# Optimization experiments

Measured on AMD Instinct MI355X. Metric: run time of the kernel, lower is better.

Reference implementation:

```python
import jax, jax.numpy as jnp
import numpy as np

N = 50000
E = 800000
D_IN = 128
D_HID = 128
D_OUT = 128
EPS = 1e-5


def setup_inputs() -> dict:
    key = jax.random.key(0)
    ks = jax.random.split(key, 10)
    x = jax.random.normal(ks[0], (N, D_IN), dtype=jnp.float32)
    edge_index = jax.random.randint(ks[1], (2, E), 0, N, dtype=jnp.int64)
    def lin(k, fi, fo):
        return jax.random.normal(k, (fi, fo), dtype=jnp.float32) / jnp.sqrt(jnp.float32(fi))
    return {
        "x": x,
        "edge_index": edge_index,
        "W1": lin(ks[2], D_IN, D_HID), "b1": jnp.zeros((D_HID,), jnp.float32),
        "W2": lin(ks[3], D_HID, D_HID), "b2": jnp.zeros((D_HID,), jnp.float32),
        "W3": lin(ks[4], D_HID, D_OUT), "b3": jnp.zeros((D_OUT,), jnp.float32),
        "g1": jnp.ones((D_HID,), jnp.float32), "be1": jnp.zeros((D_HID,), jnp.float32),
        "g2": jnp.ones((D_HID,), jnp.float32), "be2": jnp.zeros((D_HID,), jnp.float32),
    }


def _gcn_conv(x, src, dst, norm, W, b):
    # x' = D^{-1/2}(A+I)D^{-1/2} X W + b  (PyG GCNConv with self-loops)
    h = x @ W                              # [N, F]
    msgs = h[src] * norm[:, None]          # [E+N, F] gather
    agg = jax.ops.segment_sum(msgs, dst, num_segments=x.shape[0])  # scatter-add
    return agg + b


def _batchnorm(x, gamma, beta):
    mu = jnp.mean(x, axis=0)
    var = jnp.mean((x - mu) ** 2, axis=0)  # biased var, as in torch BN
    return (x - mu) * jax.lax.rsqrt(var + EPS) * gamma + beta


def reference(x, edge_index, W1, b1, W2, b2, W3, b3, g1, be1, g2, be2):
    n = x.shape[0]
    loops = jnp.arange(n, dtype=edge_index.dtype)
    src = jnp.concatenate([edge_index[0], loops])
    dst = jnp.concatenate([edge_index[1], loops])
    deg = jax.ops.segment_sum(jnp.ones_like(dst, dtype=x.dtype), dst, num_segments=n)
    dinv = jnp.where(deg > 0, jax.lax.rsqrt(deg), 0.0)
    norm = dinv[src] * dinv[dst]           # [E+N]

    h = _gcn_conv(x, src, dst, norm, W1, b1)
    h = jax.nn.relu(_batchnorm(h, g1, be1))
    h = _gcn_conv(h, src, dst, norm, W2, b2)
    h = jax.nn.relu(_batchnorm(h, g2, be2))
    h = _gcn_conv(h, src, dst, norm, W3, b3)
    # F.normalize(p=2, dim=-1)
    return h / jnp.maximum(jnp.linalg.norm(h, axis=-1, keepdims=True), 1e-12)
```

## Files before the change

### kernel.cpp

```cpp
#include <hip/hip_runtime.h>
#include <hip/hip_bf16.h>

#define D 128

typedef __bf16 bf16x8 __attribute__((ext_vector_type(8)));
typedef float floatx4 __attribute__((ext_vector_type(4)));


__global__ void k_count(const int* __restrict__ dst, int E, int* __restrict__ cnt) {
    int e = blockIdx.x * blockDim.x + threadIdx.x;
    if (e < E) atomicAdd(&cnt[dst[e]], 1);
}

__global__ __launch_bounds__(256) void k_scan1(const int* __restrict__ cnt, int n,
                                               int* __restrict__ bsum) {
    int i = blockIdx.x * 256 + threadIdx.x;
    int x = (i < n) ? cnt[i] : 0;
    #pragma unroll
    for (int off = 32; off > 0; off >>= 1) x += __shfl_xor(x, off, 64);
    __shared__ int ws[4];
    if ((threadIdx.x & 63) == 0) ws[threadIdx.x >> 6] = x;
    __syncthreads();
    if (threadIdx.x == 0) bsum[blockIdx.x] = ws[0] + ws[1] + ws[2] + ws[3];
}

__global__ void k_scan2(const int* __restrict__ bsum, int nb, int* __restrict__ boff) {
    int t = threadIdx.x;
    int lane = t & 63, wid = t >> 6;
    int x = (t < nb) ? bsum[t] : 0;
    int incl = x;
    #pragma unroll
    for (int off = 1; off < 64; off <<= 1) {
        int y = __shfl_up(incl, off, 64);
        if (lane >= off) incl += y;
    }
    __shared__ int ws[4];
    if (lane == 63) ws[wid] = incl;
    __syncthreads();
    int o = 0;
    for (int w = 0; w < wid; w++) o += ws[w];
    if (t < nb) boff[t] = o + incl - x;
}

__global__ __launch_bounds__(256) void k_scan3(const int* __restrict__ cnt,
                                               const int* __restrict__ boff, int n, int E,
                                               int* __restrict__ row_ptr, int* __restrict__ cursor,
                                               float* __restrict__ dinv) {
    int t = threadIdx.x;
    int lane = t & 63, wid = t >> 6;
    int i = blockIdx.x * 256 + t;
    int x = (i < n) ? cnt[i] : 0;
    int incl = x;
    #pragma unroll
    for (int off = 1; off < 64; off <<= 1) {
        int y = __shfl_up(incl, off, 64);
        if (lane >= off) incl += y;
    }
    __shared__ int ws[4];
    if (lane == 63) ws[wid] = incl;
    __syncthreads();
    int o = boff[blockIdx.x];
    for (int w = 0; w < wid; w++) o += ws[w];
    if (i < n) {
        int excl = o + incl - x;
        row_ptr[i] = excl;
        cursor[i] = excl;
        dinv[i] = rsqrtf((float)(x + 1));
    }
    if (blockIdx.x == 0 && t == 0) row_ptr[n] = E;
}

__global__ __launch_bounds__(256) void k_fill(const int* __restrict__ src,
                                              const int* __restrict__ dst, int E,
                                              int* __restrict__ cursor,
                                              unsigned short* __restrict__ esrc, int n) {
    int rs = (n + 7) >> 3;
    int lo = blockIdx.y * rs, hi = lo + rs;
    int step = gridDim.x * 256;
    for (int e = blockIdx.x * 256 + threadIdx.x; e < E; e += step) {
        int d = dst[e];
        int s = src[e];
        if (d >= lo && d < hi) {
            int p = atomicAdd(&cursor[d], 1);
            esrc[p] = (unsigned short)s;
        }
    }
}


__global__ __launch_bounds__(256) void k_prepw(const float* __restrict__ W1,
                                               const float* __restrict__ W2,
                                               const float* __restrict__ W3,
                                               unsigned short* __restrict__ Wt) {
    const float* W = (blockIdx.x == 0) ? W1 : (blockIdx.x == 1) ? W2 : W3;
    unsigned short* o = Wt + blockIdx.x * 16384;
    for (int i = threadIdx.x; i < 16384; i += 256) {
        int k = i >> 7, nn = i & 127;
        __hip_bfloat16 h = __float2bfloat16(W[i]);
        o[nn * 128 + k] = *(unsigned short*)&h;
    }
}


__global__ __launch_bounds__(256) void k_gemm(
    const float* __restrict__ X, const unsigned short* __restrict__ Wt,
    const float* __restrict__ scale, const float* __restrict__ stats_in,
    const float* __restrict__ gamma, const float* __restrict__ beta,
    float* __restrict__ stats_zero,
    unsigned* __restrict__ hs, int n, float invN) {
    __shared__ unsigned short Wl[128 * 128];
    __shared__ float bnl[256];
    int t = threadIdx.x;
    if (stats_in && t < 128) {
        float s = stats_in[t] + stats_in[256 + t] + stats_in[512 + t] + stats_in[768 + t];
        float q = stats_in[128 + t] + stats_in[384 + t] + stats_in[640 + t] + stats_in[896 + t];
        float mean = s * invN;
        float var = q * invN - mean * mean;
        float a = gamma[t] * rsqrtf(var + 1e-5f);
        bnl[t] = a;
        bnl[128 + t] = beta[t] - mean * a;
    }
    if (stats_zero && blockIdx.x == 0) {
        stats_zero[t] = 0.f;
        stats_zero[256 + t] = 0.f;
        stats_zero[512 + t] = 0.f;
        stats_zero[768 + t] = 0.f;
    }
    {
        const uint4* wg = (const uint4*)Wt;
        uint4* wl4 = (uint4*)Wl;
        #pragma unroll
        for (int j = 0; j < 8; j++) {
            int idx = j * 256 + t;
            int nn = idx >> 4, lc = idx & 15;
            wl4[nn * 16 + (lc ^ (nn & 15))] = wg[idx];
        }
    }
    __syncthreads();

    int l = t & 63, w = t >> 6;
    int lm = l & 15, quad = l >> 4;
    int m = blockIdx.x * 64 + w * 16 + lm;
    int rm = (m < n) ? m : (n - 1);
    const float* xrow = X + (size_t)rm * D;

    floatx4 acc[8];
    #pragma unroll
    for (int nt = 0; nt < 8; nt++) acc[nt] = (floatx4){0.f, 0.f, 0.f, 0.f};

    #pragma unroll
    for (int ks = 0; ks < 4; ks++) {
        int k0 = ks * 32 + quad * 8;
        float4 xa = *(const float4*)(xrow + k0);
        float4 xb = *(const float4*)(xrow + k0 + 4);
        if (stats_in) {
            float4 a0 = *(const float4*)&bnl[k0];
            float4 a1 = *(const float4*)&bnl[k0 + 4];
            float4 c0 = *(const float4*)&bnl[128 + k0];
            float4 c1 = *(const float4*)&bnl[128 + k0 + 4];
            xa.x = fmaxf(xa.x * a0.x + c0.x, 0.f);
            xa.y = fmaxf(xa.y * a0.y + c0.y, 0.f);
            xa.z = fmaxf(xa.z * a0.z + c0.z, 0.f);
            xa.w = fmaxf(xa.w * a0.w + c0.w, 0.f);
            xb.x = fmaxf(xb.x * a1.x + c1.x, 0.f);
            xb.y = fmaxf(xb.y * a1.y + c1.y, 0.f);
            xb.z = fmaxf(xb.z * a1.z + c1.z, 0.f);
            xb.w = fmaxf(xb.w * a1.w + c1.w, 0.f);
        }
        bf16x8 xf;
        xf[0] = (__bf16)xa.x; xf[1] = (__bf16)xa.y;
        xf[2] = (__bf16)xa.z; xf[3] = (__bf16)xa.w;
        xf[4] = (__bf16)xb.x; xf[5] = (__bf16)xb.y;
        xf[6] = (__bf16)xb.z; xf[7] = (__bf16)xb.w;
        int pc = (ks * 4 + quad) ^ lm;
        #pragma unroll
        for (int nt = 0; nt < 8; nt++) {
            const bf16x8 wf = *(const bf16x8*)&Wl[(nt * 16 + lm) * 128 + pc * 8];
            acc[nt] = __builtin_amdgcn_mfma_f32_16x16x32_bf16(wf, xf, acc[nt], 0, 0, 0);
        }
    }

    float s = scale[rm];
    if (m < n) {
        #pragma unroll
        for (int nt = 0; nt < 8; nt++) {
            __hip_bfloat16 h0 = __float2bfloat16(acc[nt][0] * s);
            __hip_bfloat16 h1 = __float2bfloat16(acc[nt][1] * s);
            __hip_bfloat16 h2 = __float2bfloat16(acc[nt][2] * s);
            __hip_bfloat16 h3 = __float2bfloat16(acc[nt][3] * s);
            uint2 uu;
            uu.x = (unsigned)*(unsigned short*)&h0 | ((unsigned)*(unsigned short*)&h1 << 16);
            uu.y = (unsigned)*(unsigned short*)&h2 | ((unsigned)*(unsigned short*)&h3 << 16);
            *(uint2*)&hs[((size_t)(nt >> 1) * n + m) * 16 + (nt & 1) * 8 + quad * 2] = uu;
        }
    }
}


__device__ inline float2 bf2f(unsigned u) {
    union { unsigned i; float f; } lo, hi;
    lo.i = u << 16;
    hi.i = u & 0xffff0000u;
    float2 r; r.x = lo.f; r.y = hi.f; return r;
}

__global__ __launch_bounds__(256) void k_agg(
    const unsigned* __restrict__ hs, const int* __restrict__ row_ptr,
    const unsigned short* __restrict__ esrc, const float* __restrict__ dinv,
    const float* __restrict__ bias, float* __restrict__ out,
    float* __restrict__ stats4, int n, int mode) {
    __shared__ float lsS[16][32];
    __shared__ float lsQ[16][32];
    int t = threadIdx.x;
    int grp = t >> 4, sub = t & 15;
    int qd = sub >> 2;
    int qe = sub & 3;
    int bid = blockIdx.x;
    int p = (bid >> 1) & 3;
    int nblk = (bid >> 3) * 2 + (bid & 1);
    const unsigned* hsp = hs + (size_t)p * n * 16;

    lsS[t >> 5][t & 31] = 0.f;
    lsS[(t >> 5) + 8][t & 31] = 0.f;
    lsQ[t >> 5][t & 31] = 0.f;
    lsQ[(t >> 5) + 8][t & 31] = 0.f;
    __syncthreads();

    float4 bA = *(const float4*)&bias[p * 32 + qe * 8];
    float4 bB = *(const float4*)&bias[p * 32 + qe * 8 + 4];

    int node0 = nblk * 64 + grp * 4;
    int rp[5];
    #pragma unroll
    for (int k = 0; k < 5; k++) {
        int ik = node0 + k;
        if (ik > n) ik = n;
        rp[k] = row_ptr[ik];
    }

    #pragma unroll
    for (int ni = 0; ni < 4; ni++) {
        int node = node0 + ni;
        if (node >= n) break;
        int beg = rp[ni], end = rp[ni + 1];
        float sc = dinv[node];
        int e_cur = (beg + sub < end) ? (int)esrc[beg + sub] : 0;
        uint4 sv = *(const uint4*)&hsp[(size_t)node * 16 + qe * 4];
        float2 a0 = bf2f(qd == 0 ? sv.x : 0u);
        float2 a1 = bf2f(qd == 0 ? sv.y : 0u);
        float2 a2 = bf2f(qd == 0 ? sv.z : 0u);
        float2 a3 = bf2f(qd == 0 ? sv.w : 0u);

        for (int base = beg; base < end; base += 16) {
            int mm = end - base;
            if (mm > 16) mm = 16;
            int e_nxt = (base + 16 + sub < end) ? (int)esrc[base + 16 + sub] : 0;
            int u0, u1, u2, u3;
            float w0, w1, w2, w3;
            {
                int ei = qd;
                int ix = ei < mm ? ei : mm - 1;
                u0 = __shfl(e_cur, ix, 16);
                w0 = ei < mm ? 1.f : 0.f;
            }
            {
                int ei = 4 + qd;
                int ix = ei < mm ? ei : mm - 1;
                u1 = __shfl(e_cur, ix, 16);
                w1 = ei < mm ? 1.f : 0.f;
            }
            {
                int ei = 8 + qd;
                int ix = ei < mm ? ei : mm - 1;
                u2 = __shfl(e_cur, ix, 16);
                w2 = ei < mm ? 1.f : 0.f;
            }
            {
                int ei = 12 + qd;
                int ix = ei < mm ? ei : mm - 1;
                u3 = __shfl(e_cur, ix, 16);
                w3 = ei < mm ? 1.f : 0.f;
            }
            uint4 g0 = *(const uint4*)&hsp[(size_t)u0 * 16 + qe * 4];
            uint4 g1 = *(const uint4*)&hsp[(size_t)u1 * 16 + qe * 4];
            uint4 g2 = *(const uint4*)&hsp[(size_t)u2 * 16 + qe * 4];
            uint4 g3 = *(const uint4*)&hsp[(size_t)u3 * 16 + qe * 4];
            float2 v;
            v = bf2f(g0.x); a0.x = fmaf(v.x, w0, a0.x); a0.y = fmaf(v.y, w0, a0.y);
            v = bf2f(g0.y); a1.x = fmaf(v.x, w0, a1.x); a1.y = fmaf(v.y, w0, a1.y);
            v = bf2f(g0.z); a2.x = fmaf(v.x, w0, a2.x); a2.y = fmaf(v.y, w0, a2.y);
            v = bf2f(g0.w); a3.x = fmaf(v.x, w0, a3.x); a3.y = fmaf(v.y, w0, a3.y);
            v = bf2f(g1.x); a0.x = fmaf(v.x, w1, a0.x); a0.y = fmaf(v.y, w1, a0.y);
            v = bf2f(g1.y); a1.x = fmaf(v.x, w1, a1.x); a1.y = fmaf(v.y, w1, a1.y);
            v = bf2f(g1.z); a2.x = fmaf(v.x, w1, a2.x); a2.y = fmaf(v.y, w1, a2.y);
            v = bf2f(g1.w); a3.x = fmaf(v.x, w1, a3.x); a3.y = fmaf(v.y, w1, a3.y);
            v = bf2f(g2.x); a0.x = fmaf(v.x, w2, a0.x); a0.y = fmaf(v.y, w2, a0.y);
            v = bf2f(g2.y); a1.x = fmaf(v.x, w2, a1.x); a1.y = fmaf(v.y, w2, a1.y);
            v = bf2f(g2.z); a2.x = fmaf(v.x, w2, a2.x); a2.y = fmaf(v.y, w2, a2.y);
            v = bf2f(g2.w); a3.x = fmaf(v.x, w2, a3.x); a3.y = fmaf(v.y, w2, a3.y);
            v = bf2f(g3.x); a0.x = fmaf(v.x, w3, a0.x); a0.y = fmaf(v.y, w3, a0.y);
            v = bf2f(g3.y); a1.x = fmaf(v.x, w3, a1.x); a1.y = fmaf(v.y, w3, a1.y);
            v = bf2f(g3.z); a2.x = fmaf(v.x, w3, a2.x); a2.y = fmaf(v.y, w3, a2.y);
            v = bf2f(g3.w); a3.x = fmaf(v.x, w3, a3.x); a3.y = fmaf(v.y, w3, a3.y);
            e_cur = e_nxt;
        }

        a0.x += __shfl_xor(a0.x, 4, 16); a0.x += __shfl_xor(a0.x, 8, 16);
        a0.y += __shfl_xor(a0.y, 4, 16); a0.y += __shfl_xor(a0.y, 8, 16);
        a1.x += __shfl_xor(a1.x, 4, 16); a1.x += __shfl_xor(a1.x, 8, 16);
        a1.y += __shfl_xor(a1.y, 4, 16); a1.y += __shfl_xor(a1.y, 8, 16);
        a2.x += __shfl_xor(a2.x, 4, 16); a2.x += __shfl_xor(a2.x, 8, 16);
        a2.y += __shfl_xor(a2.y, 4, 16); a2.y += __shfl_xor(a2.y, 8, 16);
        a3.x += __shfl_xor(a3.x, 4, 16); a3.x += __shfl_xor(a3.x, 8, 16);
        a3.y += __shfl_xor(a3.y, 4, 16); a3.y += __shfl_xor(a3.y, 8, 16);

        if (qd == 0) {
            float4 r0, r1;
            r0.x = fmaf(a0.x, sc, bA.x);
            r0.y = fmaf(a0.y, sc, bA.y);
            r0.z = fmaf(a1.x, sc, bA.z);
            r0.w = fmaf(a1.y, sc, bA.w);
            r1.x = fmaf(a2.x, sc, bB.x);
            r1.y = fmaf(a2.y, sc, bB.y);
            r1.z = fmaf(a3.x, sc, bB.z);
            r1.w = fmaf(a3.y, sc, bB.w);
            float* op = &out[(size_t)node * D + p * 32 + qe * 8];
            *(float4*)op = r0;
            *(float4*)(op + 4) = r1;
            if (mode == 0) {
                lsS[grp][qe * 8 + 0] += r0.x; lsQ[grp][qe * 8 + 0] += r0.x * r0.x;
                lsS[grp][qe * 8 + 1] += r0.y; lsQ[grp][qe * 8 + 1] += r0.y * r0.y;
                lsS[grp][qe * 8 + 2] += r0.z; lsQ[grp][qe * 8 + 2] += r0.z * r0.z;
                lsS[grp][qe * 8 + 3] += r0.w; lsQ[grp][qe * 8 + 3] += r0.w * r0.w;
                lsS[grp][qe * 8 + 4] += r1.x; lsQ[grp][qe * 8 + 4] += r1.x * r1.x;
                lsS[grp][qe * 8 + 5] += r1.y; lsQ[grp][qe * 8 + 5] += r1.y * r1.y;
                lsS[grp][qe * 8 + 6] += r1.z; lsQ[grp][qe * 8 + 6] += r1.z * r1.z;
                lsS[grp][qe * 8 + 7] += r1.w; lsQ[grp][qe * 8 + 7] += r1.w * r1.w;
            }
        }
    }

    if (mode == 0) {
        __syncthreads();
        if (t < 32) {
            float a = 0.f, c = 0.f;
            for (int g = 0; g < 16; g++) {
                a += lsS[g][t];
                c += lsQ[g][t];
            }
            float* sbuf = stats4 + ((bid >> 2) & 3) * 256;
            atomicAdd(&sbuf[p * 32 + t], a);
            atomicAdd(&sbuf[128 + p * 32 + t], c);
        }
    }
}


__global__ __launch_bounds__(256) void k_l2norm(const float* __restrict__ h,
                                                float* __restrict__ out, int n) {
    int node = blockIdx.x * 4 + (threadIdx.x >> 6);
    if (node >= n) return;
    int lane = threadIdx.x & 63;
    float2 v = *(const float2*)&h[(size_t)node * D + lane * 2];
    float pw = v.x * v.x + v.y * v.y;
    #pragma unroll
    for (int off = 32; off > 0; off >>= 1) pw += __shfl_xor(pw, off, 64);
    float sc = 1.0f / fmaxf(sqrtf(pw), 1e-12f);
    float2 r;
    r.x = v.x * sc;
    r.y = v.y * sc;
    *(float2*)&out[(size_t)node * D + lane * 2] = r;
}


extern "C" void kernel_launch(void* const* d_in, const int* in_sizes, int n_in,
                              void* d_out, int out_size, void* d_ws, size_t ws_size,
                              hipStream_t stream) {
    const float* x  = (const float*)d_in[0];
    const int*   ei = (const int*)d_in[1];
    const float* W1 = (const float*)d_in[2];
    const float* b1 = (const float*)d_in[3];
    const float* W2 = (const float*)d_in[4];
    const float* b2 = (const float*)d_in[5];
    const float* W3 = (const float*)d_in[6];
    const float* b3 = (const float*)d_in[7];
    const float* g1 = (const float*)d_in[8];
    const float* be1 = (const float*)d_in[9];
    const float* g2 = (const float*)d_in[10];
    const float* be2 = (const float*)d_in[11];

    const int N = in_sizes[0] / D;
    const int E = in_sizes[1] / 2;
    const int* src = ei;
    const int* dst = ei + E;
    const float invN = 1.0f / (float)N;

    float* Y       = (float*)d_ws;
    unsigned short* hs = (unsigned short*)(Y + (size_t)N * D);
    float* dinv    = (float*)(hs + (size_t)N * D);
    float* statsA  = dinv + N;
    float* statsB  = statsA + 1024;
    unsigned short* wt = (unsigned short*)(statsB + 1024);
    int*   cnt     = (int*)(wt + 3 * 16384);
    int*   row_ptr = cnt + N;
    int*   cursor  = row_ptr + N + 1;
    int*   bsum    = cursor + N;
    int*   boff    = bsum + 256;
    unsigned short* esrc = (unsigned short*)(boff + 256);

    const int TB = 256;
    const int gE = (E + TB - 1) / TB;
    const int NB = (N + 255) / 256;
    const int gGemm = (N + 63) / 64;
    dim3 gFill(112, 8);
    const int gx = (N + 63) / 64;
    const int gxp = (gx + 1) & ~1;
    dim3 gAgg(gxp * 4);
    const int gNode = (N + 3) / 4;

    k_prepw<<<3, TB, 0, stream>>>(W1, W2, W3, wt);
    hipMemsetAsync(cnt, 0, (size_t)N * sizeof(int), stream);
    k_count<<<gE, TB, 0, stream>>>(dst, E, cnt);
    k_scan1<<<NB, TB, 0, stream>>>(cnt, N, bsum);
    k_scan2<<<1, 256, 0, stream>>>(bsum, NB, boff);
    k_scan3<<<NB, TB, 0, stream>>>(cnt, boff, N, E, row_ptr, cursor, dinv);
    k_fill<<<gFill, TB, 0, stream>>>(src, dst, E, cursor, esrc, N);

    k_gemm<<<gGemm, TB, 0, stream>>>(x, wt, dinv, nullptr, nullptr, nullptr, statsA,
                                     (unsigned*)hs, N, invN);
    k_agg<<<gAgg, TB, 0, stream>>>((const unsigned*)hs, row_ptr, esrc, dinv, b1, Y,
                                   statsA, N, 0);

    k_gemm<<<gGemm, TB, 0, stream>>>(Y, wt + 16384, dinv, statsA, g1, be1, statsB,
                                     (unsigned*)hs, N, invN);
    k_agg<<<gAgg, TB, 0, stream>>>((const unsigned*)hs, row_ptr, esrc, dinv, b2, Y,
                                   statsB, N, 0);

    k_gemm<<<gGemm, TB, 0, stream>>>(Y, wt + 32768, dinv, statsB, g2, be2, nullptr,
                                     (unsigned*)hs, N, invN);
    k_agg<<<gAgg, TB, 0, stream>>>((const unsigned*)hs, row_ptr, esrc, dinv, b3, Y,
                                   nullptr, N, 1);
    k_l2norm<<<gNode, TB, 0, stream>>>(Y, (float*)d_out, N);
}
```

Measured before the change: 334.0 us.

## Use persistent atomic work queue for aggregation blocks per feature partition

The aggregation kernel moves from a static grid (one block per 64-node chunk and feature quarter) to a fixed grid of 2048 persistent blocks. Each block pulls 32-node units from a per-partition atomic counter, which the preceding GEMM kernel resets. The goal is load balancing over the irregular degree distribution and less block launch overhead. In exchange it adds two barriers and an atomic per unit, smaller units, and a dependency on the counter reset ordering between kernels.

```diff
diff --git a/kernel.cpp b/kernel.cpp
--- a/kernel.cpp
+++ b/kernel.cpp
@@ -106,7 +106,7 @@
     const float* __restrict__ X, const unsigned short* __restrict__ Wt,
     const float* __restrict__ scale, const float* __restrict__ stats_in,
     const float* __restrict__ gamma, const float* __restrict__ beta,
-    float* __restrict__ stats_zero,
+    float* __restrict__ stats_zero, int* __restrict__ wq,
     unsigned* __restrict__ hs, int n, float invN) {
     __shared__ unsigned short Wl[128 * 128];
     __shared__ float bnl[256];
@@ -120,11 +120,14 @@
         bnl[t] = a;
         bnl[128 + t] = beta[t] - mean * a;
     }
-    if (stats_zero && blockIdx.x == 0) {
-        stats_zero[t] = 0.f;
-        stats_zero[256 + t] = 0.f;
-        stats_zero[512 + t] = 0.f;
-        stats_zero[768 + t] = 0.f;
+    if (blockIdx.x == 0) {
+        if (stats_zero) {
+            stats_zero[t] = 0.f;
+            stats_zero[256 + t] = 0.f;
+            stats_zero[512 + t] = 0.f;
+            stats_zero[768 + t] = 0.f;
+        }
+        if (t < 8) wq[t] = 0;
     }
     {
         const uint4* wg = (const uint4*)Wt;
@@ -204,140 +207,153 @@
     float2 r; r.x = lo.f; r.y = hi.f; return r;
 }
 
+__device__ __forceinline__ void agg_node_w(
+    const unsigned* __restrict__ hsp, const unsigned short* __restrict__ esrc,
+    float* __restrict__ out, float (*lsS)[32], float (*lsQ)[32],
+    int node, int beg, int end, int e_cur, uint4 sv, float sc,
+    float4 bA, float4 bB, int grp, int sub, int qd, int qe, int p, int mode) {
+    float2 a0 = bf2f(qd == 0 ? sv.x : 0u);
+    float2 a1 = bf2f(qd == 0 ? sv.y : 0u);
+    float2 a2 = bf2f(qd == 0 ? sv.z : 0u);
+    float2 a3 = bf2f(qd == 0 ? sv.w : 0u);
+
+    for (int base = beg; base < end; base += 16) {
+        int mm = end - base;
+        if (mm > 16) mm = 16;
+        int e_nxt = (base + 16 + sub < end) ? (int)esrc[base + 16 + sub] : 0;
+        int u0, u1, u2, u3;
+        float w0, w1, w2, w3;
+        {
+            int ei = qd;
+            int ix = ei < mm ? ei : mm - 1;
+            u0 = __shfl(e_cur, ix, 16);
+            w0 = ei < mm ? 1.f : 0.f;
+        }
+        {
+            int ei = 4 + qd;
+            int ix = ei < mm ? ei : mm - 1;
+            u1 = __shfl(e_cur, ix, 16);
+            w1 = ei < mm ? 1.f : 0.f;
+        }
+        {
+            int ei = 8 + qd;
+            int ix = ei < mm ? ei : mm - 1;
+            u2 = __shfl(e_cur, ix, 16);
+            w2 = ei < mm ? 1.f : 0.f;
+        }
+        {
+            int ei = 12 + qd;
+            int ix = ei < mm ? ei : mm - 1;
+            u3 = __shfl(e_cur, ix, 16);
+            w3 = ei < mm ? 1.f : 0.f;
+        }
+        uint4 g0 = *(const uint4*)&hsp[(size_t)u0 * 16 + qe * 4];
+        uint4 g1 = *(const uint4*)&hsp[(size_t)u1 * 16 + qe * 4];
+        uint4 g2 = *(const uint4*)&hsp[(size_t)u2 * 16 + qe * 4];
+        uint4 g3 = *(const uint4*)&hsp[(size_t)u3 * 16 + qe * 4];
+        float2 v;
+        v = bf2f(g0.x); a0.x = fmaf(v.x, w0, a0.x); a0.y = fmaf(v.y, w0, a0.y);
+        v = bf2f(g0.y); a1.x = fmaf(v.x, w0, a1.x); a1.y = fmaf(v.y, w0, a1.y);
+        v = bf2f(g0.z); a2.x = fmaf(v.x, w0, a2.x); a2.y = fmaf(v.y, w0, a2.y);
+        v = bf2f(g0.w); a3.x = fmaf(v.x, w0, a3.x); a3.y = fmaf(v.y, w0, a3.y);
+        v = bf2f(g1.x); a0.x = fmaf(v.x, w1, a0.x); a0.y = fmaf(v.y, w1, a0.y);
+        v = bf2f(g1.y); a1.x = fmaf(v.x, w1, a1.x); a1.y = fmaf(v.y, w1, a1.y);
+        v = bf2f(g1.z); a2.x = fmaf(v.x, w1, a2.x); a2.y = fmaf(v.y, w1, a2.y);
+        v = bf2f(g1.w); a3.x = fmaf(v.x, w1, a3.x); a3.y = fmaf(v.y, w1, a3.y);
+        v = bf2f(g2.x); a0.x = fmaf(v.x, w2, a0.x); a0.y = fmaf(v.y, w2, a0.y);
+        v = bf2f(g2.y); a1.x = fmaf(v.x, w2, a1.x); a1.y = fmaf(v.y, w2, a1.y);
+        v = bf2f(g2.z); a2.x = fmaf(v.x, w2, a2.x); a2.y = fmaf(v.y, w2, a2.y);
+        v = bf2f(g2.w); a3.x = fmaf(v.x, w2, a3.x); a3.y = fmaf(v.y, w2, a3.y);
+        v = bf2f(g3.x); a0.x = fmaf(v.x, w3, a0.x); a0.y = fmaf(v.y, w3, a0.y);
+        v = bf2f(g3.y); a1.x = fmaf(v.x, w3, a1.x); a1.y = fmaf(v.y, w3, a1.y);
+        v = bf2f(g3.z); a2.x = fmaf(v.x, w3, a2.x); a2.y = fmaf(v.y, w3, a2.y);
+        v = bf2f(g3.w); a3.x = fmaf(v.x, w3, a3.x); a3.y = fmaf(v.y, w3, a3.y);
+        e_cur = e_nxt;
+    }
+
+    a0.x += __shfl_xor(a0.x, 4, 16); a0.x += __shfl_xor(a0.x, 8, 16);
+    a0.y += __shfl_xor(a0.y, 4, 16); a0.y += __shfl_xor(a0.y, 8, 16);
+    a1.x += __shfl_xor(a1.x, 4, 16); a1.x += __shfl_xor(a1.x, 8, 16);
+    a1.y += __shfl_xor(a1.y, 4, 16); a1.y += __shfl_xor(a1.y, 8, 16);
+    a2.x += __shfl_xor(a2.x, 4, 16); a2.x += __shfl_xor(a2.x, 8, 16);
+    a2.y += __shfl_xor(a2.y, 4, 16); a2.y += __shfl_xor(a2.y, 8, 16);
+    a3.x += __shfl_xor(a3.x, 4, 16); a3.x += __shfl_xor(a3.x, 8, 16);
+    a3.y += __shfl_xor(a3.y, 4, 16); a3.y += __shfl_xor(a3.y, 8, 16);
+
+    if (qd == 0) {
+        float4 r0, r1;
+        r0.x = fmaf(a0.x, sc, bA.x);
+        r0.y = fmaf(a0.y, sc, bA.y);
+        r0.z = fmaf(a1.x, sc, bA.z);
+        r0.w = fmaf(a1.y, sc, bA.w);
+        r1.x = fmaf(a2.x, sc, bB.x);
+        r1.y = fmaf(a2.y, sc, bB.y);
+        r1.z = fmaf(a3.x, sc, bB.z);
+        r1.w = fmaf(a3.y, sc, bB.w);
+        float* op = &out[(size_t)node * D + p * 32 + qe * 8];
+        *(float4*)op = r0;
+        *(float4*)(op + 4) = r1;
+        if (mode == 0) {
+            lsS[grp][qe * 8 + 0] += r0.x; lsQ[grp][qe * 8 + 0] += r0.x * r0.x;
+            lsS[grp][qe * 8 + 1] += r0.y; lsQ[grp][qe * 8 + 1] += r0.y * r0.y;
+            lsS[grp][qe * 8 + 2] += r0.z; lsQ[grp][qe * 8 + 2] += r0.z * r0.z;
+            lsS[grp][qe * 8 + 3] += r0.w; lsQ[grp][qe * 8 + 3] += r0.w * r0.w;
+            lsS[grp][qe * 8 + 4] += r1.x; lsQ[grp][qe * 8 + 4] += r1.x * r1.x;
+            lsS[grp][qe * 8 + 5] += r1.y; lsQ[grp][qe * 8 + 5] += r1.y * r1.y;
+            lsS[grp][qe * 8 + 6] += r1.z; lsQ[grp][qe * 8 + 6] += r1.z * r1.z;
+            lsS[grp][qe * 8 + 7] += r1.w; lsQ[grp][qe * 8 + 7] += r1.w * r1.w;
+        }
+    }
+}
+
 __global__ __launch_bounds__(256) void k_agg(
     const unsigned* __restrict__ hs, const int* __restrict__ row_ptr,
     const unsigned short* __restrict__ esrc, const float* __restrict__ dinv,
     const float* __restrict__ bias, float* __restrict__ out,
-    float* __restrict__ stats4, int n, int mode) {
+    float* __restrict__ stats4, int* __restrict__ wq, int n, int nunits, int mode) {
     __shared__ float lsS[16][32];
     __shared__ float lsQ[16][32];
+    __shared__ int snb;
     int t = threadIdx.x;
     int grp = t >> 4, sub = t & 15;
     int qd = sub >> 2;
     int qe = sub & 3;
     int bid = blockIdx.x;
-    int p = (bid >> 1) & 3;
-    int nblk = (bid >> 3) * 2 + (bid & 1);
+    int p = (bid & 7) >> 1;
     const unsigned* hsp = hs + (size_t)p * n * 16;
 
     lsS[t >> 5][t & 31] = 0.f;
     lsS[(t >> 5) + 8][t & 31] = 0.f;
     lsQ[t >> 5][t & 31] = 0.f;
     lsQ[(t >> 5) + 8][t & 31] = 0.f;
-    __syncthreads();
 
     float4 bA = *(const float4*)&bias[p * 32 + qe * 8];
     float4 bB = *(const float4*)&bias[p * 32 + qe * 8 + 4];
 
-    int node0 = nblk * 64 + grp * 4;
-    int rp[5];
-    #pragma unroll
-    for (int k = 0; k < 5; k++) {
-        int ik = node0 + k;
-        if (ik > n) ik = n;
-        rp[k] = row_ptr[ik];
-    }
-
-    #pragma unroll
-    for (int ni = 0; ni < 4; ni++) {
-        int node = node0 + ni;
-        if (node >= n) break;
-        int beg = rp[ni], end = rp[ni + 1];
-        float sc = dinv[node];
-        int e_cur = (beg + sub < end) ? (int)esrc[beg + sub] : 0;
-        uint4 sv = *(const uint4*)&hsp[(size_t)node * 16 + qe * 4];
-        float2 a0 = bf2f(qd == 0 ? sv.x : 0u);
-        float2 a1 = bf2f(qd == 0 ? sv.y : 0u);
-        float2 a2 = bf2f(qd == 0 ? sv.z : 0u);
-        float2 a3 = bf2f(qd == 0 ? sv.w : 0u);
-
-        for (int base = beg; base < end; base += 16) {
-            int mm = end - base;
-            if (mm > 16) mm = 16;
-            int e_nxt = (base + 16 + sub < end) ? (int)esrc[base + 16 + sub] : 0;
-            int u0, u1, u2, u3;
-            float w0, w1, w2, w3;
-            {
-                int ei = qd;
-                int ix = ei < mm ? ei : mm - 1;
-                u0 = __shfl(e_cur, ix, 16);
-                w0 = ei < mm ? 1.f : 0.f;
-            }
-            {
-                int ei = 4 + qd;
-                int ix = ei < mm ? ei : mm - 1;
-                u1 = __shfl(e_cur, ix, 16);
-                w1 = ei < mm ? 1.f : 0.f;
-            }
-            {
-                int ei = 8 + qd;
-                int ix = ei < mm ? ei : mm - 1;
-                u2 = __shfl(e_cur, ix, 16);
-                w2 = ei < mm ? 1.f : 0.f;
-            }
-            {
-                int ei = 12 + qd;
-                int ix = ei < mm ? ei : mm - 1;
-                u3 = __shfl(e_cur, ix, 16);
-                w3 = ei < mm ? 1.f : 0.f;
-            }
-            uint4 g0 = *(const uint4*)&hsp[(size_t)u0 * 16 + qe * 4];
-            uint4 g1 = *(const uint4*)&hsp[(size_t)u1 * 16 + qe * 4];
-            uint4 g2 = *(const uint4*)&hsp[(size_t)u2 * 16 + qe * 4];
-            uint4 g3 = *(const uint4*)&hsp[(size_t)u3 * 16 + qe * 4];
-            float2 v;
-            v = bf2f(g0.x); a0.x = fmaf(v.x, w0, a0.x); a0.y = fmaf(v.y, w0, a0.y);
-            v = bf2f(g0.y); a1.x = fmaf(v.x, w0, a1.x); a1.y = fmaf(v.y, w0, a1.y);
-            v = bf2f(g0.z); a2.x = fmaf(v.x, w0, a2.x); a2.y = fmaf(v.y, w0, a2.y);
-            v = bf2f(g0.w); a3.x = fmaf(v.x, w0, a3.x); a3.y = fmaf(v.y, w0, a3.y);
-            v = bf2f(g1.x); a0.x = fmaf(v.x, w1, a0.x); a0.y = fmaf(v.y, w1, a0.y);
-            v = bf2f(g1.y); a1.x = fmaf(v.x, w1, a1.x); a1.y = fmaf(v.y, w1, a1.y);
-            v = bf2f(g1.z); a2.x = fmaf(v.x, w1, a2.x); a2.y = fmaf(v.y, w1, a2.y);
-            v = bf2f(g1.w); a3.x = fmaf(v.x, w1, a3.x); a3.y = fmaf(v.y, w1, a3.y);
-            v = bf2f(g2.x); a0.x = fmaf(v.x, w2, a0.x); a0.y = fmaf(v.y, w2, a0.y);
-            v = bf2f(g2.y); a1.x = fmaf(v.x, w2, a1.x); a1.y = fmaf(v.y, w2, a1.y);
-            v = bf2f(g2.z); a2.x = fmaf(v.x, w2, a2.x); a2.y = fmaf(v.y, w2, a2.y);
-            v = bf2f(g2.w); a3.x = fmaf(v.x, w2, a3.x); a3.y = fmaf(v.y, w2, a3.y);
-            v = bf2f(g3.x); a0.x = fmaf(v.x, w3, a0.x); a0.y = fmaf(v.y, w3, a0.y);
-            v = bf2f(g3.y); a1.x = fmaf(v.x, w3, a1.x); a1.y = fmaf(v.y, w3, a1.y);
-            v = bf2f(g3.z); a2.x = fmaf(v.x, w3, a2.x); a2.y = fmaf(v.y, w3, a2.y);
-            v = bf2f(g3.w); a3.x = fmaf(v.x, w3, a3.x); a3.y = fmaf(v.y, w3, a3.y);
-            e_cur = e_nxt;
-        }
-
-        a0.x += __shfl_xor(a0.x, 4, 16); a0.x += __shfl_xor(a0.x, 8, 16);
-        a0.y += __shfl_xor(a0.y, 4, 16); a0.y += __shfl_xor(a0.y, 8, 16);
-        a1.x += __shfl_xor(a1.x, 4, 16); a1.x += __shfl_xor(a1.x, 8, 16);
-        a1.y += __shfl_xor(a1.y, 4, 16); a1.y += __shfl_xor(a1.y, 8, 16);
-        a2.x += __shfl_xor(a2.x, 4, 16); a2.x += __shfl_xor(a2.x, 8, 16);
-        a2.y += __shfl_xor(a2.y, 4, 16); a2.y += __shfl_xor(a2.y, 8, 16);
-        a3.x += __shfl_xor(a3.x, 4, 16); a3.x += __shfl_xor(a3.x, 8, 16);
-        a3.y += __shfl_xor(a3.y, 4, 16); a3.y += __shfl_xor(a3.y, 8, 16);
-
-        if (qd == 0) {
-            float4 r0, r1;
-            r0.x = fmaf(a0.x, sc, bA.x);
-            r0.y = fmaf(a0.y, sc, bA.y);
-            r0.z = fmaf(a1.x, sc, bA.z);
-            r0.w = fmaf(a1.y, sc, bA.w);
-            r1.x = fmaf(a2.x, sc, bB.x);
-            r1.y = fmaf(a2.y, sc, bB.y);
-            r1.z = fmaf(a3.x, sc, bB.z);
-            r1.w = fmaf(a3.y, sc, bB.w);
-            float* op = &out[(size_t)node * D + p * 32 + qe * 8];
-            *(float4*)op = r0;
-            *(float4*)(op + 4) = r1;
-            if (mode == 0) {
-                lsS[grp][qe * 8 + 0] += r0.x; lsQ[grp][qe * 8 + 0] += r0.x * r0.x;
-                lsS[grp][qe * 8 + 1] += r0.y; lsQ[grp][qe * 8 + 1] += r0.y * r0.y;
-                lsS[grp][qe * 8 + 2] += r0.z; lsQ[grp][qe * 8 + 2] += r0.z * r0.z;
-                lsS[grp][qe * 8 + 3] += r0.w; lsQ[grp][qe * 8 + 3] += r0.w * r0.w;
-                lsS[grp][qe * 8 + 4] += r1.x; lsQ[grp][qe * 8 + 4] += r1.x * r1.x;
-                lsS[grp][qe * 8 + 5] += r1.y; lsQ[grp][qe * 8 + 5] += r1.y * r1.y;
-                lsS[grp][qe * 8 + 6] += r1.z; lsQ[grp][qe * 8 + 6] += r1.z * r1.z;
-                lsS[grp][qe * 8 + 7] += r1.w; lsQ[grp][qe * 8 + 7] += r1.w * r1.w;
-            }
-        }
+    for (;;) {
+        __syncthreads();
+        if (t == 0) snb = atomicAdd(&wq[p], 1);
+        __syncthreads();
+        int unit = snb;
+        if (unit >= nunits) break;
+        int node0 = unit * 32 + grp * 2;
+        int i0 = node0 < n ? node0 : n;
+        int i1 = node0 + 1 < n ? node0 + 1 : n;
+        int i2 = node0 + 2 < n ? node0 + 2 : n;
+        int rp0 = row_ptr[i0], rp1 = row_ptr[i1], rp2 = row_ptr[i2];
+        int c0 = node0 < n ? node0 : n - 1;
+        int c1 = node0 + 1 < n ? node0 + 1 : n - 1;
+        int eA = (rp0 + sub < rp1) ? (int)esrc[rp0 + sub] : 0;
+        int eB = (rp1 + sub < rp2) ? (int)esrc[rp1 + sub] : 0;
+        uint4 svA = *(const uint4*)&hsp[(size_t)c0 * 16 + qe * 4];
+        uint4 svB = *(const uint4*)&hsp[(size_t)c1 * 16 + qe * 4];
+        float dvA = dinv[c0], dvB = dinv[c1];
+        if (node0 < n)
+            agg_node_w(hsp, esrc, out, lsS, lsQ, node0, rp0, rp1, eA, svA, dvA,
+                       bA, bB, grp, sub, qd, qe, p, mode);
+        if (node0 + 1 < n)
+            agg_node_w(hsp, esrc, out, lsS, lsQ, node0 + 1, rp1, rp2, eB, svB, dvB,
+                       bA, bB, grp, sub, qd, qe, p, mode);
     }
 
     if (mode == 0) {
@@ -406,16 +422,16 @@
     int*   cursor  = row_ptr + N + 1;
     int*   bsum    = cursor + N;
     int*   boff    = bsum + 256;
-    unsigned short* esrc = (unsigned short*)(boff + 256);
+    int*   wq      = boff + 256;
+    unsigned short* esrc = (unsigned short*)(wq + 8);
 
     const int TB = 256;
     const int gE = (E + TB - 1) / TB;
     const int NB = (N + 255) / 256;
     const int gGemm = (N + 63) / 64;
     dim3 gFill(112, 8);
-    const int gx = (N + 63) / 64;
-    const int gxp = (gx + 1) & ~1;
-    dim3 gAgg(gxp * 4);
+    const int gAgg = 2048;
+    const int aggUnits = (N + 31) / 32;
     const int gNode = (N + 3) / 4;
 
     k_prepw<<<3, TB, 0, stream>>>(W1, W2, W3, wt);
@@ -427,18 +443,18 @@
     k_fill<<<gFill, TB, 0, stream>>>(src, dst, E, cursor, esrc, N);
 
     k_gemm<<<gGemm, TB, 0, stream>>>(x, wt, dinv, nullptr, nullptr, nullptr, statsA,
-                                     (unsigned*)hs, N, invN);
+                                     wq, (unsigned*)hs, N, invN);
     k_agg<<<gAgg, TB, 0, stream>>>((const unsigned*)hs, row_ptr, esrc, dinv, b1, Y,
-                                   statsA, N, 0);
+                                   statsA, wq, N, aggUnits, 0);
 
     k_gemm<<<gGemm, TB, 0, stream>>>(Y, wt + 16384, dinv, statsA, g1, be1, statsB,
-                                     (unsigned*)hs, N, invN);
+                                     wq, (unsigned*)hs, N, invN);
     k_agg<<<gAgg, TB, 0, stream>>>((const unsigned*)hs, row_ptr, esrc, dinv, b2, Y,
-                                   statsB, N, 0);
+                                   statsB, wq, N, aggUnits, 0);
 
     k_gemm<<<gGemm, TB, 0, stream>>>(Y, wt + 32768, dinv, statsB, g2, be2, nullptr,
-                                     (unsigned*)hs, N, invN);
+                                     wq, (unsigned*)hs, N, invN);
     k_agg<<<gAgg, TB, 0, stream>>>((const unsigned*)hs, row_ptr, esrc, dinv, b3, Y,
-                                   nullptr, N, 1);
+                                   nullptr, wq, N, aggUnits, 1);
     k_l2norm<<<gNode, TB, 0, stream>>>(Y, (float*)d_out, N);
 }
```

Result: slower. 537.2 us (+60.9%).
